# Kernel tuning notes

Hardware: AMD Instinct MI355X
Metric: run time of the kernel (lower is better)

## Reference

```python
import jax, jax.numpy as jnp
import numpy as np

K = 7           # kernel_size
GROUPS = 16     # channels // group_channels = 256 // 16
GC = 16         # group_channels
BN_EPS = 1e-5


def setup_inputs() -> dict:
    key = jax.random.key(0)
    ks = jax.random.split(key, 6)
    B, C, H, W = 4, 256, 64, 64
    cr = C // 4                      # reduction_ratio = 4
    k2g = K * K * GROUPS             # conv2 out channels = 784
    return {
        "feature_map": jax.random.normal(ks[0], (B, C, H, W), jnp.float32),
        "guide_map":   jax.random.normal(ks[1], (B, C, H, W), jnp.float32),
        "w1": jax.random.normal(ks[2], (cr, C), jnp.float32) * 0.05,
        "bn_gamma": jnp.ones((cr,), jnp.float32),
        "bn_beta":  jnp.zeros((cr,), jnp.float32),
        "bn_mean":  jax.random.normal(ks[3], (cr,), jnp.float32) * 0.1,
        "bn_var":   jax.random.uniform(ks[4], (cr,), jnp.float32, 0.5, 1.5),
        "w2": jax.random.normal(ks[5], (k2g, cr), jnp.float32) * 0.05,
        "b2": jnp.zeros((k2g,), jnp.float32),
    }


def reference(feature_map, guide_map, w1, bn_gamma, bn_beta, bn_mean, bn_var, w2, b2):
    b, c, h, w = feature_map.shape
    # conv1 (1x1) + BN (inference stats) + ReLU
    x = jnp.einsum("oc,bchw->bohw", w1, guide_map)
    inv = bn_gamma / jnp.sqrt(bn_var + BN_EPS)
    x = x * inv[None, :, None, None] + (bn_beta - bn_mean * inv)[None, :, None, None]
    x = jax.nn.relu(x)
    # conv2 (1x1): dynamic per-pixel kernel weights -> [b, groups, k^2, h, w]
    weight = jnp.einsum("oc,bchw->bohw", w2, x) + b2[None, :, None, None]
    weight = weight.reshape(b, GROUPS, K * K, h, w)
    # unfold feature_map (same padding, stride 1) -> [b, c, k^2, h, w]
    pad = (K - 1) // 2
    fp = jnp.pad(feature_map, ((0, 0), (0, 0), (pad, pad), (pad, pad)))
    patches = jnp.stack(
        [fp[:, :, i:i + h, j:j + w] for i in range(K) for j in range(K)], axis=2
    )
    patches = patches.reshape(b, GROUPS, GC, K * K, h, w)
    # dynamic weighted aggregation over kernel positions, then residual
    out = jnp.einsum("bgkhw,bgckhw->bgchw", weight, patches)
    return out.reshape(b, c, h, w) + feature_map
```

## Files before the change

kernel.cpp:

```cpp
#include <hip/hip_runtime.h>

#define BN_EPS 1e-5f

typedef __bf16 bf16_t;
typedef __bf16 bf16x8 __attribute__((ext_vector_type(8)));
typedef __bf16 bf16x2 __attribute__((ext_vector_type(2)));
typedef float  floatx4 __attribute__((ext_vector_type(4)));

#define MFMA16(a, b, c) __builtin_amdgcn_mfma_f32_16x16x32_bf16((a), (b), (c), 0, 0, 0)

static __device__ __forceinline__ bf16_t f2b(float f) { return (bf16_t)f; }

#define K1P 264

__global__ __launch_bounds__(256) void conv1_mfma(
    const float* __restrict__ guide, const float* __restrict__ w1,
    const float* __restrict__ gamma, const float* __restrict__ beta,
    const float* __restrict__ mean,  const float* __restrict__ var,
    bf16_t* __restrict__ xT)
{
    __shared__ __attribute__((aligned(16))) bf16_t w1s[64 * K1P];
    __shared__ __attribute__((aligned(16))) bf16_t gTs[64 * K1P];

    const int b = blockIdx.x >> 6;
    const int h = blockIdx.x & 63;
    const int t = threadIdx.x;

#pragma unroll
    for (int i = 0; i < 16; ++i) {
        const int idx = i * 256 + t;
        const int o = idx >> 6, cq = idx & 63;
        const float4 v = *(const float4*)(w1 + o * 256 + cq * 4);
        bf16_t* d = &w1s[o * K1P + cq * 4];
        d[0] = f2b(v.x); d[1] = f2b(v.y); d[2] = f2b(v.z); d[3] = f2b(v.w);
    }
#pragma unroll
    for (int i = 0; i < 32; ++i) {
        const int idx = i * 256 + t;
        const int c2 = idx >> 6, p = idx & 63;
        const float g0 = guide[(size_t)(b * 256 + 2 * c2) * 4096 + h * 64 + p];
        const float g1 = guide[(size_t)(b * 256 + 2 * c2 + 1) * 4096 + h * 64 + p];
        bf16x2 pk; pk[0] = f2b(g0); pk[1] = f2b(g1);
        *(bf16x2*)&gTs[p * K1P + 2 * c2] = pk;
    }
    __syncthreads();

    const int wv = t >> 6;
    const int ln = t & 63;
    const int l15 = ln & 15, q = ln >> 4;

    floatx4 acc[4] = {};
    const bf16_t* ap = &w1s[(wv * 16 + l15) * K1P];
    const bf16_t* bp = &gTs[l15 * K1P];
#pragma unroll
    for (int ks = 0; ks < 8; ++ks) {
        const bf16x8 a = *(const bf16x8*)(ap + ks * 32 + q * 8);
#pragma unroll
        for (int nt = 0; nt < 4; ++nt) {
            const bf16x8 bb = *(const bf16x8*)(bp + nt * 16 * K1P + ks * 32 + q * 8);
            acc[nt] = MFMA16(a, bb, acc[nt]);
        }
    }

    float inv4[4], bia4[4];
#pragma unroll
    for (int j = 0; j < 4; ++j) {
        const int o = wv * 16 + q * 4 + j;
        const float iv = gamma[o] * rsqrtf(var[o] + BN_EPS);
        inv4[j] = iv;
        bia4[j] = beta[o] - mean[o] * iv;
    }
#pragma unroll
    for (int nt = 0; nt < 4; ++nt) {
        const int pc = nt * 16 + l15;
        bf16_t* d = xT + ((size_t)b * 4096 + h * 64 + pc) * 64 + wv * 16 + q * 4;
#pragma unroll
        for (int j = 0; j < 4; ++j) {
            const float v = fmaf(acc[nt][j], inv4[j], bia4[j]);
            d[j] = f2b(fmaxf(v, 0.f));
        }
    }
}

#define XSP 72
#define W2P 72
#define WGP 132

__global__ __launch_bounds__(256) void conv2_mfma_agg(
    const bf16_t* __restrict__ xT, const float* __restrict__ w2,
    const float* __restrict__ b2,  const float* __restrict__ feat,
    float* __restrict__ out)
{
    __shared__ __attribute__((aligned(16))) bf16_t xsT[128 * XSP];
    __shared__ __attribute__((aligned(16))) bf16_t w2s[64 * W2P];
    __shared__ __attribute__((aligned(16))) float  wgs[49 * WGP];

    const int gq = blockIdx.x & 3;
    const int bh = blockIdx.x >> 2;
    const int b  = bh >> 5;
    const int h0 = (bh & 31) * 2;
    const int t  = threadIdx.x;

    {
        const bf16_t* src = xT + ((size_t)b * 4096 + h0 * 64) * 64;
#pragma unroll
        for (int i = 0; i < 4; ++i) {
            const int u = i * 256 + t;
            const int p = u >> 3, cq = u & 7;
            *(uint4*)&xsT[p * XSP + cq * 8] = *(const uint4*)(src + p * 64 + cq * 8);
        }
    }

    for (int gi = 0; gi < 4; ++gi) {
        const int g = gq * 4 + gi;
        if (gi) __syncthreads();

#pragma unroll
        for (int i = 0; i < 4; ++i) {
            const int u = i * 256 + t;
            const int k = u >> 4, cq = u & 15;
            float4 v = {0.f, 0.f, 0.f, 0.f};
            if (k < 49) v = *(const float4*)(w2 + (size_t)(g * 49 + k) * 64 + cq * 4);
            bf16_t* d = &w2s[k * W2P + cq * 4];
            d[0] = f2b(v.x); d[1] = f2b(v.y); d[2] = f2b(v.z); d[3] = f2b(v.w);
        }
        __syncthreads();

        {
            const int wv = t >> 6, ln = t & 63;
            const int l15 = ln & 15, q = ln >> 4;
            floatx4 acc[8] = {};
            const bf16_t* ap = &w2s[(wv * 16 + l15) * W2P];
            const bf16x8 a0 = *(const bf16x8*)(ap + q * 8);
            const bf16x8 a1 = *(const bf16x8*)(ap + 32 + q * 8);
#pragma unroll
            for (int nt = 0; nt < 8; ++nt) {
                const bf16_t* bp = &xsT[(nt * 16 + l15) * XSP + q * 8];
                acc[nt] = MFMA16(a0, *(const bf16x8*)(bp), acc[nt]);
                acc[nt] = MFMA16(a1, *(const bf16x8*)(bp + 32), acc[nt]);
            }
            const int krow = wv * 16 + q * 4;
            float bias[4];
#pragma unroll
            for (int j = 0; j < 4; ++j)
                bias[j] = (krow + j < 49) ? b2[g * 49 + krow + j] : 0.f;
#pragma unroll
            for (int nt = 0; nt < 8; ++nt) {
                const int pc = nt * 16 + l15;
#pragma unroll
                for (int j = 0; j < 4; ++j) {
                    const int k = krow + j;
                    if (k < 49) wgs[k * WGP + pc] = acc[nt][j] + bias[j];
                }
            }
        }
        __syncthreads();

        {
            const int wq = t & 15;
            const int r  = (t >> 4) & 1;
            const int cp = t >> 5;
            const int w0 = wq * 4;
            const int ch0 = g * 16 + cp * 2;
            const int hr = h0 + r;

            float acc0[4] = {0.f, 0.f, 0.f, 0.f};
            float acc1[4] = {0.f, 0.f, 0.f, 0.f};
#pragma unroll
            for (int di = 0; di < 7; ++di) {
                const int hh = hr + di - 3;
                if (hh < 0 || hh >= 64) continue;
                const float* fp0 = feat + ((size_t)(b * 256 + ch0) * 64 + hh) * 64;
                const float* fp1 = fp0 + 4096;
                float f0[10], f1[10];
#pragma unroll
                for (int j = 0; j < 10; ++j) {
                    const int ww = w0 - 3 + j;
                    const bool ok = (ww >= 0) && (ww < 64);
                    f0[j] = ok ? fp0[ww] : 0.f;
                    f1[j] = ok ? fp1[ww] : 0.f;
                }
                const float* wrow = &wgs[(di * 7) * WGP + r * 64 + w0];
#pragma unroll
                for (int dj = 0; dj < 7; ++dj) {
                    const floatx4 wv4 = *(const floatx4*)(wrow + dj * WGP);
#pragma unroll
                    for (int x = 0; x < 4; ++x) {
                        acc0[x] = fmaf(wv4[x], f0[x + dj], acc0[x]);
                        acc1[x] = fmaf(wv4[x], f1[x + dj], acc1[x]);
                    }
                }
            }
            const size_t ob = ((size_t)(b * 256 + ch0) * 64 + hr) * 64 + w0;
            const float4 r0 = *(const float4*)(feat + ob);
            const float4 r1 = *(const float4*)(feat + ob + 4096);
            float4 o0, o1;
            o0.x = acc0[0] + r0.x; o0.y = acc0[1] + r0.y; o0.z = acc0[2] + r0.z; o0.w = acc0[3] + r0.w;
            o1.x = acc1[0] + r1.x; o1.y = acc1[1] + r1.y; o1.z = acc1[2] + r1.z; o1.w = acc1[3] + r1.w;
            *(float4*)(out + ob) = o0;
            *(float4*)(out + ob + 4096) = o1;
        }
    }
}

extern "C" void kernel_launch(void* const* d_in, const int* in_sizes, int n_in,
                              void* d_out, int out_size, void* d_ws, size_t ws_size,
                              hipStream_t stream) {
    const float* feature = (const float*)d_in[0];
    const float* guide   = (const float*)d_in[1];
    const float* w1      = (const float*)d_in[2];
    const float* gamma   = (const float*)d_in[3];
    const float* beta    = (const float*)d_in[4];
    const float* mean    = (const float*)d_in[5];
    const float* var     = (const float*)d_in[6];
    const float* w2      = (const float*)d_in[7];
    const float* b2      = (const float*)d_in[8];
    float* out = (float*)d_out;
    bf16_t* xT = (bf16_t*)d_ws;

    conv1_mfma<<<4 * 64, 256, 0, stream>>>(guide, w1, gamma, beta, mean, var, xT);
    conv2_mfma_agg<<<4 * 32 * 4, 256, 0, stream>>>(xT, w2, b2, feature, out);
}
```

Before: 150.3 us.

## Fuse conv1 into the aggregation kernel with a bf16 weight-prep pass

Replaces the separate conv1 kernel and its global xT intermediate with a tiny prep kernel that folds the BN scale into bf16 w1 and converts w2 to bf16. A single fused kernel then computes conv1 per block straight from the guide map into LDS. It also stores the dynamic weights as bf16 in LDS, uses float4 feature loads, and splits groups across 8 blocks per row pair. The cost is that each block recomputes conv1 for its two rows, eight times per row pair, and reads guide with strided scalar loads. The bf16 dynamic weights also lower precision.

```diff
diff --git a/kernel.cpp b/kernel.cpp
--- a/kernel.cpp
+++ b/kernel.cpp
@@ -4,199 +4,175 @@
 
 typedef __bf16 bf16_t;
 typedef __bf16 bf16x8 __attribute__((ext_vector_type(8)));
-typedef __bf16 bf16x2 __attribute__((ext_vector_type(2)));
+typedef __bf16 bf16x4 __attribute__((ext_vector_type(4)));
 typedef float  floatx4 __attribute__((ext_vector_type(4)));
 
 #define MFMA16(a, b, c) __builtin_amdgcn_mfma_f32_16x16x32_bf16((a), (b), (c), 0, 0, 0)
 
-static __device__ __forceinline__ bf16_t f2b(float f) { return (bf16_t)f; }
-
-#define K1P 264
-
-__global__ __launch_bounds__(256) void conv1_mfma(
-    const float* __restrict__ guide, const float* __restrict__ w1,
-    const float* __restrict__ gamma, const float* __restrict__ beta,
-    const float* __restrict__ mean,  const float* __restrict__ var,
-    bf16_t* __restrict__ xT)
+#define W1B_OFF 0
+#define W2B_OFF 32768
+#define B1_OFF  133120
+
+__global__ __launch_bounds__(256) void prep(
+    const float* __restrict__ w1, const float* __restrict__ gamma,
+    const float* __restrict__ beta, const float* __restrict__ mean,
+    const float* __restrict__ var, const float* __restrict__ w2,
+    bf16_t* __restrict__ w1b, bf16_t* __restrict__ w2b, float* __restrict__ bias1)
 {
-    __shared__ __attribute__((aligned(16))) bf16_t w1s[64 * K1P];
-    __shared__ __attribute__((aligned(16))) bf16_t gTs[64 * K1P];
-
-    const int b = blockIdx.x >> 6;
-    const int h = blockIdx.x & 63;
-    const int t = threadIdx.x;
-
-#pragma unroll
-    for (int i = 0; i < 16; ++i) {
-        const int idx = i * 256 + t;
-        const int o = idx >> 6, cq = idx & 63;
-        const float4 v = *(const float4*)(w1 + o * 256 + cq * 4);
-        bf16_t* d = &w1s[o * K1P + cq * 4];
-        d[0] = f2b(v.x); d[1] = f2b(v.y); d[2] = f2b(v.z); d[3] = f2b(v.w);
-    }
-#pragma unroll
-    for (int i = 0; i < 32; ++i) {
-        const int idx = i * 256 + t;
-        const int c2 = idx >> 6, p = idx & 63;
-        const float g0 = guide[(size_t)(b * 256 + 2 * c2) * 4096 + h * 64 + p];
-        const float g1 = guide[(size_t)(b * 256 + 2 * c2 + 1) * 4096 + h * 64 + p];
-        bf16x2 pk; pk[0] = f2b(g0); pk[1] = f2b(g1);
-        *(bf16x2*)&gTs[p * K1P + 2 * c2] = pk;
-    }
-    __syncthreads();
-
-    const int wv = t >> 6;
-    const int ln = t & 63;
-    const int l15 = ln & 15, q = ln >> 4;
-
-    floatx4 acc[4] = {};
-    const bf16_t* ap = &w1s[(wv * 16 + l15) * K1P];
-    const bf16_t* bp = &gTs[l15 * K1P];
-#pragma unroll
-    for (int ks = 0; ks < 8; ++ks) {
-        const bf16x8 a = *(const bf16x8*)(ap + ks * 32 + q * 8);
-#pragma unroll
-        for (int nt = 0; nt < 4; ++nt) {
-            const bf16x8 bb = *(const bf16x8*)(bp + nt * 16 * K1P + ks * 32 + q * 8);
-            acc[nt] = MFMA16(a, bb, acc[nt]);
-        }
-    }
-
-    float inv4[4], bia4[4];
-#pragma unroll
-    for (int j = 0; j < 4; ++j) {
-        const int o = wv * 16 + q * 4 + j;
-        const float iv = gamma[o] * rsqrtf(var[o] + BN_EPS);
-        inv4[j] = iv;
-        bia4[j] = beta[o] - mean[o] * iv;
-    }
-#pragma unroll
-    for (int nt = 0; nt < 4; ++nt) {
-        const int pc = nt * 16 + l15;
-        bf16_t* d = xT + ((size_t)b * 4096 + h * 64 + pc) * 64 + wv * 16 + q * 4;
-#pragma unroll
-        for (int j = 0; j < 4; ++j) {
-            const float v = fmaf(acc[nt][j], inv4[j], bia4[j]);
-            d[j] = f2b(fmaxf(v, 0.f));
-        }
+    const int idx = blockIdx.x * 256 + threadIdx.x;
+    if (idx < 16384) {
+        const int o = idx >> 8;
+        const float inv = gamma[o] * rsqrtf(var[o] + BN_EPS);
+        w1b[idx] = (bf16_t)(w1[idx] * inv);
+        if (idx < 64) {
+            const float iv = gamma[idx] * rsqrtf(var[idx] + BN_EPS);
+            bias1[idx] = beta[idx] - mean[idx] * iv;
+        }
+    } else if (idx < 16384 + 50176) {
+        const int j = idx - 16384;
+        w2b[j] = (bf16_t)w2[j];
     }
 }
 
 #define XSP 72
-#define W2P 72
 #define WGP 132
 
-__global__ __launch_bounds__(256) void conv2_mfma_agg(
-    const bf16_t* __restrict__ xT, const float* __restrict__ w2,
-    const float* __restrict__ b2,  const float* __restrict__ feat,
+__global__ __launch_bounds__(256, 4) void fused(
+    const float* __restrict__ guide, const bf16_t* __restrict__ w1b,
+    const float* __restrict__ bias1, const bf16_t* __restrict__ w2b,
+    const float* __restrict__ b2,    const float* __restrict__ feat,
     float* __restrict__ out)
 {
     __shared__ __attribute__((aligned(16))) bf16_t xsT[128 * XSP];
-    __shared__ __attribute__((aligned(16))) bf16_t w2s[64 * W2P];
-    __shared__ __attribute__((aligned(16))) float  wgs[49 * WGP];
-
-    const int gq = blockIdx.x & 3;
-    const int bh = blockIdx.x >> 2;
+    __shared__ __attribute__((aligned(16))) bf16_t wgs[49 * WGP];
+
+    const int gp = blockIdx.x & 7;
+    const int bh = blockIdx.x >> 3;
     const int b  = bh >> 5;
     const int h0 = (bh & 31) * 2;
     const int t  = threadIdx.x;
+    const int wv = t >> 6, ln = t & 63, l15 = ln & 15, q = ln >> 4;
 
     {
-        const bf16_t* src = xT + ((size_t)b * 4096 + h0 * 64) * 64;
-#pragma unroll
-        for (int i = 0; i < 4; ++i) {
-            const int u = i * 256 + t;
-            const int p = u >> 3, cq = u & 7;
-            *(uint4*)&xsT[p * XSP + cq * 8] = *(const uint4*)(src + p * 64 + cq * 8);
+        floatx4 acc[4][2] = {};
+        const float* gbase = guide + (size_t)b * 256 * 4096 + h0 * 64;
+        for (int ks = 0; ks < 8; ++ks) {
+            bf16x8 bf[2];
+#pragma unroll
+            for (int nt = 0; nt < 2; ++nt) {
+                const int p = wv * 32 + nt * 16 + l15;
+                const float* gpp = gbase + (size_t)(ks * 32 + q * 8) * 4096 + p;
+                bf16x8 v;
+#pragma unroll
+                for (int j = 0; j < 8; ++j) v[j] = (bf16_t)gpp[(size_t)j * 4096];
+                bf[nt] = v;
+            }
+#pragma unroll
+            for (int mt = 0; mt < 4; ++mt) {
+                const bf16x8 a = *(const bf16x8*)(w1b + (mt * 16 + l15) * 256 + ks * 32 + q * 8);
+                acc[mt][0] = MFMA16(a, bf[0], acc[mt][0]);
+                acc[mt][1] = MFMA16(a, bf[1], acc[mt][1]);
+            }
+        }
+#pragma unroll
+        for (int mt = 0; mt < 4; ++mt) {
+            float bi[4];
+#pragma unroll
+            for (int j = 0; j < 4; ++j) bi[j] = bias1[mt * 16 + q * 4 + j];
+#pragma unroll
+            for (int nt = 0; nt < 2; ++nt) {
+                const int p = wv * 32 + nt * 16 + l15;
+                bf16x4 v;
+#pragma unroll
+                for (int j = 0; j < 4; ++j)
+                    v[j] = (bf16_t)fmaxf(acc[mt][nt][j] + bi[j], 0.f);
+                *(bf16x4*)&xsT[p * XSP + mt * 16 + q * 4] = v;
+            }
         }
     }
-
-    for (int gi = 0; gi < 4; ++gi) {
-        const int g = gq * 4 + gi;
+    __syncthreads();
+
+    for (int gi = 0; gi < 2; ++gi) {
+        const int g = gp * 2 + gi;
         if (gi) __syncthreads();
 
-#pragma unroll
-        for (int i = 0; i < 4; ++i) {
-            const int u = i * 256 + t;
-            const int k = u >> 4, cq = u & 15;
-            float4 v = {0.f, 0.f, 0.f, 0.f};
-            if (k < 49) v = *(const float4*)(w2 + (size_t)(g * 49 + k) * 64 + cq * 4);
-            bf16_t* d = &w2s[k * W2P + cq * 4];
-            d[0] = f2b(v.x); d[1] = f2b(v.y); d[2] = f2b(v.z); d[3] = f2b(v.w);
+        {
+            floatx4 acc[4][2] = {};
+#pragma unroll
+            for (int ks = 0; ks < 2; ++ks) {
+                bf16x8 bfr[2];
+#pragma unroll
+                for (int nt = 0; nt < 2; ++nt) {
+                    const int p = wv * 32 + nt * 16 + l15;
+                    bfr[nt] = *(const bf16x8*)&xsT[p * XSP + ks * 32 + q * 8];
+                }
+#pragma unroll
+                for (int mt = 0; mt < 4; ++mt) {
+                    int row = g * 49 + mt * 16 + l15;
+                    row = row > 783 ? 783 : row;
+                    const bf16x8 a = *(const bf16x8*)(w2b + row * 64 + ks * 32 + q * 8);
+                    acc[mt][0] = MFMA16(a, bfr[0], acc[mt][0]);
+                    acc[mt][1] = MFMA16(a, bfr[1], acc[mt][1]);
+                }
+            }
+#pragma unroll
+            for (int mt = 0; mt < 4; ++mt) {
+#pragma unroll
+                for (int j = 0; j < 4; ++j) {
+                    const int k = mt * 16 + q * 4 + j;
+                    if (k < 49) {
+                        const float bias = b2[g * 49 + k];
+#pragma unroll
+                        for (int nt = 0; nt < 2; ++nt) {
+                            const int p = wv * 32 + nt * 16 + l15;
+                            wgs[k * WGP + p] = (bf16_t)(acc[mt][nt][j] + bias);
+                        }
+                    }
+                }
+            }
         }
         __syncthreads();
 
         {
-            const int wv = t >> 6, ln = t & 63;
-            const int l15 = ln & 15, q = ln >> 4;
-            floatx4 acc[8] = {};
-            const bf16_t* ap = &w2s[(wv * 16 + l15) * W2P];
-            const bf16x8 a0 = *(const bf16x8*)(ap + q * 8);
-            const bf16x8 a1 = *(const bf16x8*)(ap + 32 + q * 8);
-#pragma unroll
-            for (int nt = 0; nt < 8; ++nt) {
-                const bf16_t* bp = &xsT[(nt * 16 + l15) * XSP + q * 8];
-                acc[nt] = MFMA16(a0, *(const bf16x8*)(bp), acc[nt]);
-                acc[nt] = MFMA16(a1, *(const bf16x8*)(bp + 32), acc[nt]);
-            }
-            const int krow = wv * 16 + q * 4;
-            float bias[4];
-#pragma unroll
-            for (int j = 0; j < 4; ++j)
-                bias[j] = (krow + j < 49) ? b2[g * 49 + krow + j] : 0.f;
-#pragma unroll
-            for (int nt = 0; nt < 8; ++nt) {
-                const int pc = nt * 16 + l15;
-#pragma unroll
-                for (int j = 0; j < 4; ++j) {
-                    const int k = krow + j;
-                    if (k < 49) wgs[k * WGP + pc] = acc[nt][j] + bias[j];
-                }
-            }
-        }
-        __syncthreads();
-
-        {
-            const int wq = t & 15;
-            const int r  = (t >> 4) & 1;
-            const int cp = t >> 5;
+            const int wq = t & 15, r = (t >> 4) & 1, cp = t >> 5;
             const int w0 = wq * 4;
             const int ch0 = g * 16 + cp * 2;
             const int hr = h0 + r;
-
-            float acc0[4] = {0.f, 0.f, 0.f, 0.f};
-            float acc1[4] = {0.f, 0.f, 0.f, 0.f};
+            float a0[4] = {0.f, 0.f, 0.f, 0.f}, a1[4] = {0.f, 0.f, 0.f, 0.f};
 #pragma unroll
             for (int di = 0; di < 7; ++di) {
                 const int hh = hr + di - 3;
                 if (hh < 0 || hh >= 64) continue;
-                const float* fp0 = feat + ((size_t)(b * 256 + ch0) * 64 + hh) * 64;
-                const float* fp1 = fp0 + 4096;
+                const float* r0 = feat + ((size_t)(b * 256 + ch0) * 64 + hh) * 64;
+                const float* r1 = r0 + 4096;
+                float4 L0 = {0,0,0,0}, L1 = {0,0,0,0}, R0 = {0,0,0,0}, R1 = {0,0,0,0};
+                if (wq > 0)  { L0 = *(const float4*)(r0 + w0 - 4); L1 = *(const float4*)(r1 + w0 - 4); }
+                const float4 M0 = *(const float4*)(r0 + w0);
+                const float4 M1 = *(const float4*)(r1 + w0);
+                if (wq < 15) { R0 = *(const float4*)(r0 + w0 + 4); R1 = *(const float4*)(r1 + w0 + 4); }
                 float f0[10], f1[10];
-#pragma unroll
-                for (int j = 0; j < 10; ++j) {
-                    const int ww = w0 - 3 + j;
-                    const bool ok = (ww >= 0) && (ww < 64);
-                    f0[j] = ok ? fp0[ww] : 0.f;
-                    f1[j] = ok ? fp1[ww] : 0.f;
-                }
-                const float* wrow = &wgs[(di * 7) * WGP + r * 64 + w0];
+                f0[0]=L0.y; f0[1]=L0.z; f0[2]=L0.w; f0[3]=M0.x; f0[4]=M0.y;
+                f0[5]=M0.z; f0[6]=M0.w; f0[7]=R0.x; f0[8]=R0.y; f0[9]=R0.z;
+                f1[0]=L1.y; f1[1]=L1.z; f1[2]=L1.w; f1[3]=M1.x; f1[4]=M1.y;
+                f1[5]=M1.z; f1[6]=M1.w; f1[7]=R1.x; f1[8]=R1.y; f1[9]=R1.z;
+                const bf16_t* wrow = &wgs[(di * 7) * WGP + r * 64 + w0];
 #pragma unroll
                 for (int dj = 0; dj < 7; ++dj) {
-                    const floatx4 wv4 = *(const floatx4*)(wrow + dj * WGP);
+                    const bf16x4 wb = *(const bf16x4*)(wrow + dj * WGP);
 #pragma unroll
                     for (int x = 0; x < 4; ++x) {
-                        acc0[x] = fmaf(wv4[x], f0[x + dj], acc0[x]);
-                        acc1[x] = fmaf(wv4[x], f1[x + dj], acc1[x]);
+                        const float wf = (float)wb[x];
+                        a0[x] = fmaf(wf, f0[x + dj], a0[x]);
+                        a1[x] = fmaf(wf, f1[x + dj], a1[x]);
                     }
                 }
             }
             const size_t ob = ((size_t)(b * 256 + ch0) * 64 + hr) * 64 + w0;
-            const float4 r0 = *(const float4*)(feat + ob);
-            const float4 r1 = *(const float4*)(feat + ob + 4096);
+            const float4 q0 = *(const float4*)(feat + ob);
+            const float4 q1 = *(const float4*)(feat + ob + 4096);
             float4 o0, o1;
-            o0.x = acc0[0] + r0.x; o0.y = acc0[1] + r0.y; o0.z = acc0[2] + r0.z; o0.w = acc0[3] + r0.w;
-            o1.x = acc1[0] + r1.x; o1.y = acc1[1] + r1.y; o1.z = acc1[2] + r1.z; o1.w = acc1[3] + r1.w;
+            o0.x = a0[0] + q0.x; o0.y = a0[1] + q0.y; o0.z = a0[2] + q0.z; o0.w = a0[3] + q0.w;
+            o1.x = a1[0] + q1.x; o1.y = a1[1] + q1.y; o1.z = a1[2] + q1.z; o1.w = a1[3] + q1.w;
             *(float4*)(out + ob) = o0;
             *(float4*)(out + ob + 4096) = o1;
         }
@@ -216,8 +192,13 @@
     const float* w2      = (const float*)d_in[7];
     const float* b2      = (const float*)d_in[8];
     float* out = (float*)d_out;
-    bf16_t* xT = (bf16_t*)d_ws;
-
-    conv1_mfma<<<4 * 64, 256, 0, stream>>>(guide, w1, gamma, beta, mean, var, xT);
-    conv2_mfma_agg<<<4 * 32 * 4, 256, 0, stream>>>(xT, w2, b2, feature, out);
+
+    char* ws = (char*)d_ws;
+    bf16_t* w1b   = (bf16_t*)(ws + W1B_OFF);
+    bf16_t* w2b   = (bf16_t*)(ws + W2B_OFF);
+    float*  bias1 = (float*) (ws + B1_OFF);
+
+    prep<<<(16384 + 50176 + 255) / 256, 256, 0, stream>>>(
+        w1, gamma, beta, mean, var, w2, w1b, w2b, bias1);
+    fused<<<1024, 256, 0, stream>>>(guide, w1b, bias1, w2b, b2, feature, out);
 }
```

Measured after the change: 137.8 us. -8.4%, faster.
